# Optimization experiments

Hardware: AMD Instinct MI355X
Metric: run time of the kernel (lower is better)

## Reference

```python
import jax, jax.numpy as jnp
import numpy as np

N = 50000      # nodes
E = 800000     # edges
IN = 128       # in_channels
HID = 32       # hidden_channels (per-head dim)
HEADS = 4
HC = HEADS * HID  # 128
OUT = 16       # classes
B = 64         # graphs in batch


def setup_inputs() -> dict:
    key = jax.random.key(0)
    ks = jax.random.split(key, 32)
    def nrm(k, shp, scale):
        return (jax.random.normal(k, shp, jnp.float32) * scale).astype(jnp.float32)
    inp = {}
    inp["x"] = nrm(ks[0], (N, IN), 1.0)
    inp["edge_index"] = jax.random.randint(ks[1], (2, E), 0, N, dtype=jnp.int32)
    inp["edge_attr"] = nrm(ks[2], (E, HID), 1.0)
    inp["batch"] = jnp.sort(jax.random.randint(ks[3], (N,), 0, B, dtype=jnp.int32))
    s_in = IN ** -0.5
    s_hc = HC ** -0.5
    s_hid = HID ** -0.5
    # conv1: lin_query/key/value (IN->HC, bias), lin_edge (HID->HC, no bias), lin_skip (IN->HC, bias)
    inp["wq1"] = nrm(ks[4], (IN, HC), s_in);  inp["bq1"] = jnp.zeros((HC,), jnp.float32)
    inp["wk1"] = nrm(ks[5], (IN, HC), s_in);  inp["bk1"] = jnp.zeros((HC,), jnp.float32)
    inp["wv1"] = nrm(ks[6], (IN, HC), s_in);  inp["bv1"] = jnp.zeros((HC,), jnp.float32)
    inp["we1"] = nrm(ks[7], (HID, HC), s_hid)
    inp["ws1"] = nrm(ks[8], (IN, HC), s_in);  inp["bs1"] = jnp.zeros((HC,), jnp.float32)
    # conv2: input dim HC
    inp["wq2"] = nrm(ks[9], (HC, HC), s_hc);  inp["bq2"] = jnp.zeros((HC,), jnp.float32)
    inp["wk2"] = nrm(ks[10], (HC, HC), s_hc); inp["bk2"] = jnp.zeros((HC,), jnp.float32)
    inp["wv2"] = nrm(ks[11], (HC, HC), s_hc); inp["bv2"] = jnp.zeros((HC,), jnp.float32)
    inp["we2"] = nrm(ks[12], (HID, HC), s_hid)
    inp["ws2"] = nrm(ks[13], (HC, HC), s_hc); inp["bs2"] = jnp.zeros((HC,), jnp.float32)
    # final classifier
    inp["wlin"] = nrm(ks[14], (HC, OUT), s_hc); inp["blin"] = jnp.zeros((OUT,), jnp.float32)
    return inp


def _tconv(x, src, tgt, ea, wq, bq, wk, bk, wv, bv, we, ws, bs):
    """PyG TransformerConv (concat=True, root_weight=True, eval/no dropout)."""
    qn = x @ wq + bq          # [N, HC]
    kn = x @ wk + bk
    vn = x @ wv + bv
    e = ea @ we               # [E, HC] edge embedding (added to key and value)
    q = qn[tgt].reshape(E, HEADS, HID)
    k = (kn[src] + e).reshape(E, HEADS, HID)
    v = (vn[src] + e).reshape(E, HEADS, HID)
    alpha = (q * k).sum(-1) / np.float32(np.sqrt(HID))   # [E, HEADS]
    # segment softmax over target node
    m = jax.ops.segment_max(alpha, tgt, num_segments=N)  # [N, HEADS]
    a = jnp.exp(alpha - m[tgt])
    den = jax.ops.segment_sum(a, tgt, num_segments=N)
    a = a / den[tgt]
    agg = jax.ops.segment_sum(a[:, :, None] * v, tgt, num_segments=N)  # [N, HEADS, HID]
    return agg.reshape(N, HC) + (x @ ws + bs)


def reference(x, edge_index, edge_attr, batch,
              wq1, bq1, wk1, bk1, wv1, bv1, we1, ws1, bs1,
              wq2, bq2, wk2, bk2, wv2, bv2, we2, ws2, bs2,
              wlin, blin):
    src, tgt = edge_index[0], edge_index[1]
    h = jax.nn.elu(_tconv(x, src, tgt, edge_attr, wq1, bq1, wk1, bk1, wv1, bv1, we1, ws1, bs1))
    h = jax.nn.elu(_tconv(h, src, tgt, edge_attr, wq2, bq2, wk2, bk2, wv2, bv2, we2, ws2, bs2))
    # global mean pool over graphs
    s = jax.ops.segment_sum(h, batch, num_segments=B)                    # [B, HC]
    cnt = jax.ops.segment_sum(jnp.ones((N,), jnp.float32), batch, num_segments=B)
    pooled = s / jnp.maximum(cnt, 1.0)[:, None]
    logits = pooled @ wlin + blin
    return jax.nn.log_softmax(logits, axis=-1)
```

## Files before the change

kernel.cpp:

```cpp
#include <hip/hip_runtime.h>
#include <hip/hip_fp16.h>

#define N_NODES 50000
#define N_EDGES 800000
#define IN_C 128
#define HID 32
#define HC 128
#define OUT_C 16
#define NGRAPH 64
#define PNB 125
#define TPB 2
#define NPB_SCAN 1024
#define NSCAN_BLKS ((N_NODES + NPB_SCAN - 1) / NPB_SCAN)

typedef __attribute__((ext_vector_type(8))) _Float16 half8;
typedef __attribute__((ext_vector_type(4))) _Float16 half4v;
typedef __attribute__((ext_vector_type(2))) _Float16 half2v;
typedef __attribute__((ext_vector_type(4))) float floatx4;

__global__ void k_hist(const int* __restrict__ tgt, int* __restrict__ deg) {
  int i = blockIdx.x * blockDim.x + threadIdx.x;
  if (i < N_EDGES) atomicAdd(&deg[tgt[i]], 1);
}

__global__ __launch_bounds__(256) void k_scan1(const int* __restrict__ deg,
                                               int* __restrict__ bsum) {
  int i4 = blockIdx.x * 256 + threadIdx.x;
  int4 d = {0, 0, 0, 0};
  if (i4 * 4 < N_NODES) d = ((const int4*)deg)[i4];
  int s = d.x + d.y + d.z + d.w;
#pragma unroll
  for (int off = 1; off < 64; off <<= 1) s += __shfl_xor(s, off, 64);
  __shared__ int ws[4];
  int lane = threadIdx.x & 63, w = threadIdx.x >> 6;
  if (lane == 0) ws[w] = s;
  __syncthreads();
  if (threadIdx.x == 0) bsum[blockIdx.x] = ws[0] + ws[1] + ws[2] + ws[3];
}

__global__ void k_scan2(int* __restrict__ bsum) {
  int lane = threadIdx.x;
  int v = (lane < NSCAN_BLKS) ? bsum[lane] : 0;
  int x = v;
#pragma unroll
  for (int off = 1; off < 64; off <<= 1) {
    int t = __shfl_up(x, off, 64);
    if (lane >= off) x += t;
  }
  if (lane < NSCAN_BLKS) bsum[lane] = x - v;
}

__global__ __launch_bounds__(256) void k_scan3(const int* __restrict__ deg,
                                               const int* __restrict__ bbase,
                                               int* __restrict__ offs,
                                               int* __restrict__ cursor) {
  int t = threadIdx.x, lane = t & 63, w = t >> 6;
  int i4 = blockIdx.x * 256 + t;
  int4 d = {0, 0, 0, 0};
  bool valid = (i4 * 4 < N_NODES);
  if (valid) d = ((const int4*)deg)[i4];
  int s0 = d.x, s1 = s0 + d.y, s2 = s1 + d.z, s3 = s2 + d.w;
  int x = s3;
#pragma unroll
  for (int off = 1; off < 64; off <<= 1) {
    int tt = __shfl_up(x, off, 64);
    if (lane >= off) x += tt;
  }
  __shared__ int ws[4];
  if (lane == 63) ws[w] = x;
  __syncthreads();
  int wadd = 0;
  for (int k = 0; k < w; ++k) wadd += ws[k];
  int base = bbase[blockIdx.x] + wadd + (x - s3);
  if (valid) {
    int i = i4 * 4;
    int4 cur = {base, base + s0, base + s1, base + s2};
    ((int4*)&cursor[i])[0] = cur;
    offs[i + 1] = base + s0;
    offs[i + 2] = base + s1;
    offs[i + 3] = base + s2;
    offs[i + 4] = base + s3;
  }
  if (blockIdx.x == 0 && t == 0) offs[0] = 0;
}

__global__ __launch_bounds__(256) void k_scatter(
    const int* __restrict__ src, const int* __restrict__ tgt,
    int* __restrict__ cursor, const float* __restrict__ ea,
    int* __restrict__ srcs, _Float16* __restrict__ eac) {
  int i = blockIdx.x * 32 + (threadIdx.x >> 3);
  int c = threadIdx.x & 7;
  int lane = threadIdx.x & 63;
  int pos = 0;
  if (c == 0) pos = atomicAdd(&cursor[tgt[i]], 1);
  pos = __shfl(pos, lane & 0x38, 64);
  if (c == 0) srcs[pos] = src[i];
  float4 v = *(const float4*)&ea[(size_t)i * HID + c * 4];
  half4v h = {(_Float16)v.x, (_Float16)v.y, (_Float16)v.z, (_Float16)v.w};
  *(half4v*)&eac[(size_t)pos * HID + c * 4] = h;
}

__global__ __launch_bounds__(128) void k_prep_w(
    const float* __restrict__ wq, const float* __restrict__ wk,
    const float* __restrict__ wv, const float* __restrict__ ws,
    const float* __restrict__ bq, const float* __restrict__ we,
    _Float16* __restrict__ wt, float* __restrict__ bp) {
  int g = blockIdx.x;
  int k = threadIdx.x;
  if (g < 512) {
    const float* w = (g < 128) ? wq : (g < 256) ? wk : (g < 384) ? wv : ws;
    int c = g & 127;
    wt[(size_t)g * HC + k] = (_Float16)w[k * HC + c];
  } else {
    int c = g - 512;
    int hb = (c >> 5) << 5, j = c & 31;
    float s = 0.f;
#pragma unroll
    for (int d = 0; d < 32; ++d)
      s = fmaf(wq[k * HC + hb + d], we[j * HC + hb + d], s);
    wt[(size_t)g * HC + k] = (_Float16)s;
    if (k == 0) {
      float b = 0.f;
      for (int d = 0; d < 32; ++d) b = fmaf(bq[hb + d], we[j * HC + hb + d], b);
      bp[c] = b;
    }
  }
}

template <bool IN32>
__global__ __launch_bounds__(256) void k_gemm(
    const void* __restrict__ ain_,
    const _Float16* __restrict__ wt,
    const float* __restrict__ bq, const float* __restrict__ bk,
    const float* __restrict__ bv, const float* __restrict__ bs,
    const float* __restrict__ bp,
    __half* __restrict__ qn16, _Float16* __restrict__ kv16,
    _Float16* __restrict__ sk16, __half* __restrict__ p16) {
  __shared__ _Float16 Bs[128][132];
  int tid = threadIdx.x;
  int wv = tid >> 6, lane = tid & 63;
  int quad = lane >> 4, l16 = lane & 15;
  int cb = blockIdx.y;

#pragma unroll
  for (int i = 0; i < 8; ++i) {
    int chunk = i * 256 + tid;
    int col = chunk >> 4, kc16 = chunk & 15;
    half8 b = *(const half8*)&wt[(size_t)(cb * 128 + col) * HC + kc16 * 8];
    *(half8*)&Bs[col][kc16 * 8] = b;
  }

  int r0 = blockIdx.x * 128 + wv * 32;
  half8 A[2][4];
#pragma unroll
  for (int m = 0; m < 2; ++m) {
    int arow = min(r0 + m * 16 + l16, N_NODES - 1);
#pragma unroll
    for (int kc = 0; kc < 4; ++kc) {
      if constexpr (IN32) {
        const float* ain = (const float*)ain_;
        const float4* ap = (const float4*)&ain[(size_t)arow * HC + kc * 32 + quad * 8];
        float4 a0 = ap[0], a1 = ap[1];
        A[m][kc] = (half8){(_Float16)a0.x, (_Float16)a0.y, (_Float16)a0.z,
                           (_Float16)a0.w, (_Float16)a1.x, (_Float16)a1.y,
                           (_Float16)a1.z, (_Float16)a1.w};
      } else {
        const _Float16* ain = (const _Float16*)ain_;
        A[m][kc] = *(const half8*)&ain[(size_t)arow * HC + kc * 32 + quad * 8];
      }
    }
  }
  floatx4 acc[8][2];
#pragma unroll
  for (int ct = 0; ct < 8; ++ct) {
    acc[ct][0] = (floatx4){0.f, 0.f, 0.f, 0.f};
    acc[ct][1] = (floatx4){0.f, 0.f, 0.f, 0.f};
  }
  __syncthreads();

#pragma unroll
  for (int ct = 0; ct < 8; ++ct) {
#pragma unroll
    for (int kc = 0; kc < 4; ++kc) {
      half8 B = *(const half8*)&Bs[ct * 16 + l16][kc * 32 + quad * 8];
      acc[ct][0] = __builtin_amdgcn_mfma_f32_16x16x32_f16(A[0][kc], B, acc[ct][0], 0, 0, 0);
      acc[ct][1] = __builtin_amdgcn_mfma_f32_16x16x32_f16(A[1][kc], B, acc[ct][1], 0, 0, 0);
    }
  }

  const float* bias = (cb == 0) ? bq : (cb == 1) ? bk : (cb == 2) ? bv
                    : (cb == 3) ? bs : bp;
#pragma unroll
  for (int ct = 0; ct < 8; ++ct) {
    int lc = (ct << 4) + l16;
    float b = bias[lc];
#pragma unroll
    for (int m = 0; m < 2; ++m) {
#pragma unroll
      for (int reg = 0; reg < 4; ++reg) {
        int row = r0 + m * 16 + quad * 4 + reg;
        if (row < N_NODES) {
          float val = acc[ct][m][reg] + b;
          if (cb == 0) qn16[(size_t)row * HC + lc] = __float2half(val);
          else if (cb == 1) kv16[(size_t)row * 256 + lc] = (_Float16)val;
          else if (cb == 2) kv16[(size_t)row * 256 + 128 + lc] = (_Float16)val;
          else if (cb == 3) sk16[(size_t)row * HC + lc] = (_Float16)val;
          else p16[(size_t)row * HC + lc] = __float2half(val);
        }
      }
    }
  }
}

__device__ __forceinline__ float dot8(half8 a, half8 b, float c) {
#if __has_builtin(__builtin_amdgcn_fdot2)
#pragma unroll
  for (int i = 0; i < 4; ++i) {
    half2v x = {a[2 * i], a[2 * i + 1]};
    half2v y = {b[2 * i], b[2 * i + 1]};
    c = __builtin_amdgcn_fdot2(x, y, c, false);
  }
#else
#pragma unroll
  for (int i = 0; i < 8; ++i) c = fmaf((float)a[i], (float)b[i], c);
#endif
  return c;
}

__device__ __forceinline__ float quad_red(float x) {
  int b = __builtin_amdgcn_update_dpp(0, __float_as_int(x), 0xB1, 0xF, 0xF, true);
  float y = x + __int_as_float(b);
  int c2 = __builtin_amdgcn_update_dpp(0, __float_as_int(y), 0x4E, 0xF, 0xF, true);
  return y + __int_as_float(c2);
}

__global__ __launch_bounds__(128) void k_edge_attn(
    const int* __restrict__ offs, const int* __restrict__ srcs,
    const _Float16* __restrict__ eac,
    const _Float16* __restrict__ qn, const _Float16* __restrict__ kv,
    const _Float16* __restrict__ sk,
    const _Float16* __restrict__ pn, const float* __restrict__ we,
    _Float16* __restrict__ o16) {
  int lane = threadIdx.x & 63;
  int wv_ = threadIdx.x >> 6;
  int t = blockIdx.x * TPB + wv_;
  int g = lane >> 4;
  int p = lane & 15;
  int f0 = p << 3;
  int jd0 = (p & 3) << 3;

  half8 qh = *(const half8*)&qn[(size_t)t * HC + f0];
  half8 ph = *(const half8*)&pn[(size_t)t * HC + ((p >> 2) << 5) + jd0];

  int e0 = offs[t], e1 = offs[t + 1];
  const float inv_sqrt = 0.17677669529663687f;
  float den = 0.f;
  float acc[8], tac[8];
#pragma unroll
  for (int i = 0; i < 8; ++i) { acc[i] = 0.f; tac[i] = 0.f; }

  int sl = (e0 < e1) ? srcs[min(e0 + (lane & 15), e1 - 1)] : 0;
  for (int base = e0; base < e1; base += 16) {
    int cnt = e1 - base;
    half8 K[4], V[4], E[4];
#pragma unroll
    for (int i = 0; i < 4; ++i) {
      int j = 4 * g + i;
      int jc = min(j, cnt - 1);
      int s = __shfl(sl, jc, 64);
      const _Float16* kvp = &kv[(size_t)s * 256];
      K[i] = *(const half8*)&kvp[f0];
      V[i] = *(const half8*)&kvp[128 + f0];
      E[i] = *(const half8*)&eac[(size_t)(base + jc) * HID + jd0];
    }
    int nb = base + 16;
    int sl_n = (nb < e1) ? srcs[min(nb + (lane & 15), e1 - 1)] : 0;
#pragma unroll
    for (int i = 0; i < 4; ++i) {
      int j = 4 * g + i;
      float part = dot8(qh, K[i], 0.f);
      part = dot8(ph, E[i], part);
      part = quad_red(part);
      float w = (j < cnt) ? __expf(part * inv_sqrt) : 0.f;
      den += w;
#pragma unroll
      for (int q2 = 0; q2 < 8; ++q2) {
        acc[q2] = fmaf(w, (float)V[i][q2], acc[q2]);
        tac[q2] = fmaf(w, (float)E[i][q2], tac[q2]);
      }
    }
    sl = sl_n;
  }

#pragma unroll
  for (int i = 0; i < 8; ++i) {
    acc[i] += __shfl_xor(acc[i], 16, 64); acc[i] += __shfl_xor(acc[i], 32, 64);
    tac[i] += __shfl_xor(tac[i], 16, 64); tac[i] += __shfl_xor(tac[i], 32, 64);
  }
  den += __shfl_xor(den, 16, 64);
  den += __shfl_xor(den, 32, 64);

  __shared__ float tl[TPB][16][9];
  if (g == 0) {
#pragma unroll
    for (int i = 0; i < 8; ++i) tl[wv_][p][i] = tac[i];
  }
  float fx[8];
#pragma unroll
  for (int i = 0; i < 8; ++i) fx[i] = 0.f;
  int r = (p & 12) + g;
#pragma unroll
  for (int u = 0; u < 8; ++u) {
    float tv = tl[wv_][r][u];
    int j = (g << 3) + u;
    const float4* wr = (const float4*)&we[j * HC + f0];
    float4 w0 = wr[0], w1 = wr[1];
    fx[0] = fmaf(tv, w0.x, fx[0]); fx[1] = fmaf(tv, w0.y, fx[1]);
    fx[2] = fmaf(tv, w0.z, fx[2]); fx[3] = fmaf(tv, w0.w, fx[3]);
    fx[4] = fmaf(tv, w1.x, fx[4]); fx[5] = fmaf(tv, w1.y, fx[5]);
    fx[6] = fmaf(tv, w1.z, fx[6]); fx[7] = fmaf(tv, w1.w, fx[7]);
  }
#pragma unroll
  for (int i = 0; i < 8; ++i) {
    fx[i] += __shfl_xor(fx[i], 16, 64);
    fx[i] += __shfl_xor(fx[i], 32, 64);
  }

  if (g == 0) {
    float rd = (e1 > e0) ? (1.0f / den) : 0.f;
    half8 s8 = *(const half8*)&sk[(size_t)t * HC + f0];
    float o[8];
#pragma unroll
    for (int i = 0; i < 8; ++i) {
      o[i] = fmaf(acc[i] + fx[i], rd, (float)s8[i]);
      o[i] = o[i] > 0.f ? o[i] : __expf(o[i]) - 1.f;
    }
    half8 v16 = {(_Float16)o[0], (_Float16)o[1], (_Float16)o[2], (_Float16)o[3],
                 (_Float16)o[4], (_Float16)o[5], (_Float16)o[6], (_Float16)o[7]};
    *(half8*)&o16[(size_t)t * HC + f0] = v16;
  }
}

__global__ __launch_bounds__(128) void k_pool_sum(const _Float16* __restrict__ h16,
                                                  const int* __restrict__ batch,
                                                  float* __restrict__ psum) {
  int c = threadIdx.x;
  int n0 = blockIdx.x * PNB;
  int n1 = n0 + PNB;
  float acc = 0.f;
  int curb = batch[n0];
  for (int n = n0; n < n1; ++n) {
    int b = batch[n];
    if (b != curb) {
      atomicAdd(&psum[curb * HC + c], acc);
      acc = 0.f;
      curb = b;
    }
    acc += (float)h16[(size_t)n * HC + c];
  }
  atomicAdd(&psum[curb * HC + c], acc);
}

__global__ __launch_bounds__(1024) void k_classify(const float* __restrict__ psum,
                                                   const int* __restrict__ batch,
                                                   const float* __restrict__ wlin,
                                                   const float* __restrict__ blin,
                                                   float* __restrict__ out) {
  int tid = threadIdx.x;
  int b = tid >> 4, o = tid & 15;
  int lo = 0, hi = N_NODES;
  while (lo < hi) { int mid = (lo + hi) >> 1; if (batch[mid] < b) lo = mid + 1; else hi = mid; }
  int start = lo;
  lo = 0; hi = N_NODES;
  while (lo < hi) { int mid = (lo + hi) >> 1; if (batch[mid] <= b) lo = mid + 1; else hi = mid; }
  float cnt = fmaxf((float)(lo - start), 1.0f);
  float dot = 0.f;
  for (int d = 0; d < HC; ++d) dot = fmaf(psum[b * HC + d], wlin[d * OUT_C + o], dot);
  float acc = dot / cnt + blin[o];
  float mx = acc;
#pragma unroll
  for (int off = 8; off > 0; off >>= 1) mx = fmaxf(mx, __shfl_xor(mx, off, 64));
  float ex = __expf(acc - mx);
  float sum = ex;
#pragma unroll
  for (int off = 8; off > 0; off >>= 1) sum += __shfl_xor(sum, off, 64);
  out[tid] = acc - mx - logf(sum);
}

extern "C" void kernel_launch(void* const* d_in, const int* in_sizes, int n_in,
                              void* d_out, int out_size, void* d_ws, size_t ws_size,
                              hipStream_t stream) {
  const float* x = (const float*)d_in[0];
  const int* ei = (const int*)d_in[1];
  const float* ea = (const float*)d_in[2];
  const int* batch = (const int*)d_in[3];
  const float* wq1 = (const float*)d_in[4];  const float* bq1 = (const float*)d_in[5];
  const float* wk1 = (const float*)d_in[6];  const float* bk1 = (const float*)d_in[7];
  const float* wv1 = (const float*)d_in[8];  const float* bv1 = (const float*)d_in[9];
  const float* we1 = (const float*)d_in[10];
  const float* ws1 = (const float*)d_in[11]; const float* bs1 = (const float*)d_in[12];
  const float* wq2 = (const float*)d_in[13]; const float* bq2 = (const float*)d_in[14];
  const float* wk2 = (const float*)d_in[15]; const float* bk2 = (const float*)d_in[16];
  const float* wv2 = (const float*)d_in[17]; const float* bv2 = (const float*)d_in[18];
  const float* we2 = (const float*)d_in[19];
  const float* ws2 = (const float*)d_in[20]; const float* bs2 = (const float*)d_in[21];
  const float* wlin = (const float*)d_in[22]; const float* blin = (const float*)d_in[23];

  const int* srcI = ei;
  const int* tgtI = ei + N_EDGES;

  char* wsb = (char*)d_ws;
  size_t off = 0;
  auto alloc = [&](size_t bytes) -> void* {
    void* ptr = wsb + off;
    off += (bytes + 255) & ~(size_t)255;
    return ptr;
  };
  __half* qn16 = (__half*)alloc((size_t)N_NODES * HC * 2);
  _Float16* kv16 = (_Float16*)alloc((size_t)N_NODES * 256 * 2);
  __half* p16  = (__half*)alloc((size_t)N_NODES * HC * 2);
  _Float16* sk16 = (_Float16*)alloc((size_t)N_NODES * HC * 2);
  _Float16* h16 = (_Float16*)alloc((size_t)N_NODES * HC * 2);
  _Float16* in16 = (_Float16*)alloc((size_t)N_NODES * HC * 2);
  _Float16* wt1 = (_Float16*)alloc((size_t)640 * HC * 2);
  _Float16* wt2 = (_Float16*)alloc((size_t)640 * HC * 2);
  float* bp1 = (float*)alloc((size_t)HC * 4);
  float* bp2 = (float*)alloc((size_t)HC * 4);
  float* psum = (float*)alloc((size_t)NGRAPH * HC * 4);
  int* deg    = (int*)alloc((size_t)N_NODES * 4);
  int* offs   = (int*)alloc((size_t)(N_NODES + 1) * 4);
  int* cursor = (int*)alloc((size_t)N_NODES * 4);
  int* srcs   = (int*)alloc((size_t)N_EDGES * 4);
  int* bsum   = (int*)alloc((size_t)NSCAN_BLKS * 4);
  _Float16* eac = (_Float16*)alloc((size_t)N_EDGES * HID * 2);

  hipMemsetAsync(deg, 0, (size_t)N_NODES * 4, stream);
  k_hist<<<(N_EDGES + 255) / 256, 256, 0, stream>>>(tgtI, deg);
  k_scan1<<<NSCAN_BLKS, 256, 0, stream>>>(deg, bsum);
  k_scan2<<<1, 64, 0, stream>>>(bsum);
  k_scan3<<<NSCAN_BLKS, 256, 0, stream>>>(deg, bsum, offs, cursor);
  k_scatter<<<N_EDGES / 32, 256, 0, stream>>>(srcI, tgtI, cursor, ea, srcs, eac);

  k_prep_w<<<640, 128, 0, stream>>>(wq1, wk1, wv1, ws1, bq1, we1, wt1, bp1);
  k_prep_w<<<640, 128, 0, stream>>>(wq2, wk2, wv2, ws2, bq2, we2, wt2, bp2);

  dim3 gemm_grid((N_NODES + 127) / 128, 5);
  k_gemm<true><<<gemm_grid, 256, 0, stream>>>(x, wt1, bq1, bk1, bv1, bs1, bp1,
                                              qn16, kv16, sk16, p16);
  k_edge_attn<<<N_NODES / TPB, 64 * TPB, 0, stream>>>(
      offs, srcs, eac, (const _Float16*)qn16, kv16, sk16,
      (const _Float16*)p16, we1, in16);
  k_gemm<false><<<gemm_grid, 256, 0, stream>>>(in16, wt2, bq2, bk2, bv2, bs2, bp2,
                                               qn16, kv16, sk16, p16);
  k_edge_attn<<<N_NODES / TPB, 64 * TPB, 0, stream>>>(
      offs, srcs, eac, (const _Float16*)qn16, kv16, sk16,
      (const _Float16*)p16, we2, h16);

  hipMemsetAsync(psum, 0, (size_t)NGRAPH * HC * 4, stream);
  k_pool_sum<<<N_NODES / PNB, 128, 0, stream>>>(h16, batch, psum);
  k_classify<<<1, 1024, 0, stream>>>(psum, batch, wlin, blin, (float*)d_out);
}
```

Before: 619.3 us.

## Loop over all five weight blocks per GEMM block to reuse A rows

The node GEMM now has each block own 64 rows and loop over all five output column blocks (q, k, v, skip, p), reloading the weight tile into shared memory each iteration. Before, a 2D grid had separate blocks per column block, each re-reading the same 128 input rows. The change reads the input activations once instead of five times, which helps most for the fp32 first-layer input. In exchange each block does serial weight reloads with extra barriers, holds fewer rows per wave, and the grid has fewer total blocks.

```diff
diff --git a/kernel.cpp b/kernel.cpp
--- a/kernel.cpp
+++ b/kernel.cpp
@@ -140,67 +140,60 @@
   int tid = threadIdx.x;
   int wv = tid >> 6, lane = tid & 63;
   int quad = lane >> 4, l16 = lane & 15;
-  int cb = blockIdx.y;
-
-#pragma unroll
-  for (int i = 0; i < 8; ++i) {
-    int chunk = i * 256 + tid;
-    int col = chunk >> 4, kc16 = chunk & 15;
-    half8 b = *(const half8*)&wt[(size_t)(cb * 128 + col) * HC + kc16 * 8];
-    *(half8*)&Bs[col][kc16 * 8] = b;
-  }
-
-  int r0 = blockIdx.x * 128 + wv * 32;
-  half8 A[2][4];
-#pragma unroll
-  for (int m = 0; m < 2; ++m) {
-    int arow = min(r0 + m * 16 + l16, N_NODES - 1);
-#pragma unroll
-    for (int kc = 0; kc < 4; ++kc) {
-      if constexpr (IN32) {
-        const float* ain = (const float*)ain_;
-        const float4* ap = (const float4*)&ain[(size_t)arow * HC + kc * 32 + quad * 8];
-        float4 a0 = ap[0], a1 = ap[1];
-        A[m][kc] = (half8){(_Float16)a0.x, (_Float16)a0.y, (_Float16)a0.z,
-                           (_Float16)a0.w, (_Float16)a1.x, (_Float16)a1.y,
-                           (_Float16)a1.z, (_Float16)a1.w};
-      } else {
-        const _Float16* ain = (const _Float16*)ain_;
-        A[m][kc] = *(const half8*)&ain[(size_t)arow * HC + kc * 32 + quad * 8];
+
+  int r0 = blockIdx.x * 64 + wv * 16;
+  int arow = min(r0 + l16, N_NODES - 1);
+  half8 A[4];
+#pragma unroll
+  for (int kc = 0; kc < 4; ++kc) {
+    if constexpr (IN32) {
+      const float* ain = (const float*)ain_;
+      const float4* ap = (const float4*)&ain[(size_t)arow * HC + kc * 32 + quad * 8];
+      float4 a0 = ap[0], a1 = ap[1];
+      A[kc] = (half8){(_Float16)a0.x, (_Float16)a0.y, (_Float16)a0.z,
+                      (_Float16)a0.w, (_Float16)a1.x, (_Float16)a1.y,
+                      (_Float16)a1.z, (_Float16)a1.w};
+    } else {
+      const _Float16* ain = (const _Float16*)ain_;
+      A[kc] = *(const half8*)&ain[(size_t)arow * HC + kc * 32 + quad * 8];
+    }
+  }
+
+#pragma unroll
+  for (int cb = 0; cb < 5; ++cb) {
+    __syncthreads();
+#pragma unroll
+    for (int i = 0; i < 8; ++i) {
+      int chunk = i * 256 + tid;
+      int col = chunk >> 4, kc16 = chunk & 15;
+      half8 b = *(const half8*)&wt[(size_t)(cb * 128 + col) * HC + kc16 * 8];
+      *(half8*)&Bs[col][kc16 * 8] = b;
+    }
+    __syncthreads();
+
+    floatx4 acc[8];
+#pragma unroll
+    for (int ct = 0; ct < 8; ++ct) acc[ct] = (floatx4){0.f, 0.f, 0.f, 0.f};
+#pragma unroll
+    for (int ct = 0; ct < 8; ++ct) {
+#pragma unroll
+      for (int kc = 0; kc < 4; ++kc) {
+        half8 B = *(const half8*)&Bs[ct * 16 + l16][kc * 32 + quad * 8];
+        acc[ct] = __builtin_amdgcn_mfma_f32_16x16x32_f16(A[kc], B, acc[ct], 0, 0, 0);
       }
     }
-  }
-  floatx4 acc[8][2];
-#pragma unroll
-  for (int ct = 0; ct < 8; ++ct) {
-    acc[ct][0] = (floatx4){0.f, 0.f, 0.f, 0.f};
-    acc[ct][1] = (floatx4){0.f, 0.f, 0.f, 0.f};
-  }
-  __syncthreads();
-
-#pragma unroll
-  for (int ct = 0; ct < 8; ++ct) {
-#pragma unroll
-    for (int kc = 0; kc < 4; ++kc) {
-      half8 B = *(const half8*)&Bs[ct * 16 + l16][kc * 32 + quad * 8];
-      acc[ct][0] = __builtin_amdgcn_mfma_f32_16x16x32_f16(A[0][kc], B, acc[ct][0], 0, 0, 0);
-      acc[ct][1] = __builtin_amdgcn_mfma_f32_16x16x32_f16(A[1][kc], B, acc[ct][1], 0, 0, 0);
-    }
-  }
-
-  const float* bias = (cb == 0) ? bq : (cb == 1) ? bk : (cb == 2) ? bv
-                    : (cb == 3) ? bs : bp;
-#pragma unroll
-  for (int ct = 0; ct < 8; ++ct) {
-    int lc = (ct << 4) + l16;
-    float b = bias[lc];
-#pragma unroll
-    for (int m = 0; m < 2; ++m) {
+
+    const float* bias = (cb == 0) ? bq : (cb == 1) ? bk : (cb == 2) ? bv
+                      : (cb == 3) ? bs : bp;
+#pragma unroll
+    for (int ct = 0; ct < 8; ++ct) {
+      int lc = (ct << 4) + l16;
+      float b = bias[lc];
 #pragma unroll
       for (int reg = 0; reg < 4; ++reg) {
-        int row = r0 + m * 16 + quad * 4 + reg;
+        int row = r0 + quad * 4 + reg;
         if (row < N_NODES) {
-          float val = acc[ct][m][reg] + b;
+          float val = acc[ct][reg] + b;
           if (cb == 0) qn16[(size_t)row * HC + lc] = __float2half(val);
           else if (cb == 1) kv16[(size_t)row * 256 + lc] = (_Float16)val;
           else if (cb == 2) kv16[(size_t)row * 256 + 128 + lc] = (_Float16)val;
@@ -444,7 +437,7 @@
   k_prep_w<<<640, 128, 0, stream>>>(wq1, wk1, wv1, ws1, bq1, we1, wt1, bp1);
   k_prep_w<<<640, 128, 0, stream>>>(wq2, wk2, wv2, ws2, bq2, we2, wt2, bp2);
 
-  dim3 gemm_grid((N_NODES + 127) / 128, 5);
+  int gemm_grid = (N_NODES + 63) / 64;
   k_gemm<true><<<gemm_grid, 256, 0, stream>>>(x, wt1, bq1, bk1, bv1, bs1, bp1,
                                               qn16, kv16, sk16, p16);
   k_edge_attn<<<N_NODES / TPB, 64 * TPB, 0, stream>>>(
```

Result: faster. 564.7 us (-8.8%).
